# Performance work log

Measured on AMD Instinct MI355X. Metric: run time of the kernel, lower is better.

Reference implementation:

```python
import jax, jax.numpy as jnp
import numpy as np

N_NODES = 50000
N_EDGES = 600000
N_RELS = 19
D_IN = 128
D_HID = 64
D_OUT = 2


def setup_inputs() -> dict:
    key = jax.random.key(0)
    ks = jax.random.split(key, 10)
    feat = jax.random.normal(ks[0], (N_NODES, D_IN), dtype=jnp.float32)
    src = jax.random.randint(ks[1], (N_EDGES,), 0, N_NODES)
    dst = jax.random.randint(ks[2], (N_EDGES,), 0, N_NODES)
    etype = jax.random.randint(ks[3], (N_EDGES,), 0, N_RELS)
    s1 = 1.0 / np.sqrt(D_IN)
    s2 = 1.0 / np.sqrt(D_HID)
    W1 = jax.random.normal(ks[4], (N_RELS, D_IN, D_HID), dtype=jnp.float32) * s1
    loop1 = jax.random.normal(ks[5], (D_IN, D_HID), dtype=jnp.float32) * s1
    b1 = jnp.zeros((D_HID,), dtype=jnp.float32)
    W2 = jax.random.normal(ks[6], (N_RELS, D_HID, D_OUT), dtype=jnp.float32) * s2
    loop2 = jax.random.normal(ks[7], (D_HID, D_OUT), dtype=jnp.float32) * s2
    b2 = jnp.zeros((D_OUT,), dtype=jnp.float32)
    return {"feat": feat, "W1": W1, "loop1": loop1, "b1": b1,
            "W2": W2, "loop2": loop2, "b2": b2,
            "src": src, "dst": dst, "etype": etype}


def _rel_graph_conv(h, W, loop_w, bias, src, dst, etype, activation):
    # Per-relation transform of all nodes: [N, R, O]; then gather per edge.
    # (num_rels * out_feat is small, so this is cheaper than gathering W per edge.)
    transformed = jnp.einsum('nd,rdo->nro', h, W)
    msg = transformed[src, etype]                      # [E, O] edge messages
    agg = jax.ops.segment_sum(msg, dst, num_segments=h.shape[0])  # scatter-add
    out = agg + h @ loop_w + bias                      # self-loop + bias
    if activation is not None:
        out = activation(out)
    return out


def reference(feat, W1, loop1, b1, W2, loop2, b2, src, dst, etype):
    h = _rel_graph_conv(feat, W1, loop1, b1, src, dst, etype, jax.nn.relu)
    h = _rel_graph_conv(h, W2, loop2, b2, src, dst, etype, None)
    return h
```

## Files before the change

kernel.cpp:

```cpp
#include <hip/hip_runtime.h>

#define N_NODES 50000
#define N_EDGES 600000
#define N_RELS  19
#define D_IN    128
#define D_HID   64
#define D_OUT   2
#define BSH     9
#define NB      ((N_NODES + 511) >> 9)
#define NSEG    (NB * N_RELS)
#define NTILE_CAP (NSEG + (N_EDGES + 127) / 128)
#define SL_BLOCKS  ((N_NODES + 63) / 64)
#define PREP_ELEMS (N_RELS * D_HID * D_IN + 48 * 64 + D_HID * D_IN)
#define PREP_BLOCKS ((PREP_ELEMS + 255) / 256)

typedef unsigned short u16;
typedef unsigned int   u32;
typedef __attribute__((ext_vector_type(8))) short sfrag;
typedef __attribute__((ext_vector_type(4))) float f32x4;

__device__ __forceinline__ u16 f2bf(float f){
  union { float f; u32 i; } v; v.f = f;
  u32 r = v.i + 0x7fffu + ((v.i >> 16) & 1u);
  return (u16)(r >> 16);
}
__device__ __forceinline__ float bf2f(u16 u){
  union { u32 i; float f; } v; v.i = ((u32)u) << 16; return v.f;
}
__device__ __forceinline__ u32 pack2(float lo, float hi){
  return (u32)f2bf(lo) | ((u32)f2bf(hi) << 16);
}

__global__ __launch_bounds__(256) void k_fused_pre(const float* __restrict__ feat,
                                                   u16* __restrict__ featb,
                                                   const int* __restrict__ src,
                                                   const int* __restrict__ et,
                                                   const int* __restrict__ dst,
                                                   int* __restrict__ seg_hist,
                                                   int* __restrict__ hist_dst){
  int i = blockIdx.x * 256 + threadIdx.x;
  float2 f = ((const float2*)feat)[i];
  ((u32*)featb)[i] = (u32)f2bf(f.x) | ((u32)f2bf(f.y) << 16);
  if (i < N_EDGES) {
    int key = (src[i] >> BSH) * N_RELS + et[i];
    atomicAdd(&seg_hist[key * 16], 1);
    atomicAdd(&hist_dst[dst[i]], 1);
  }
}

__global__ __launch_bounds__(256) void k_alloc_scan(
    const int* __restrict__ hist_dst, int* __restrict__ dstart,
    int* __restrict__ cur_dst, int* __restrict__ gcnt,
    const int* __restrict__ seg_hist, int* __restrict__ seg_off,
    int* __restrict__ cur_seg, int* __restrict__ ntile,
    int* __restrict__ tseg, int* __restrict__ tstart,
    const float* __restrict__ W1, const float* __restrict__ loop1,
    const float* __restrict__ W2, u16* __restrict__ W1Tb,
    u16* __restrict__ loop1Tb, u16* __restrict__ W2allT){
  if (blockIdx.x >= 197) {
    int idx = (blockIdx.x - 197) * 256 + threadIdx.x;
    const int T1 = N_RELS * D_HID * D_IN;
    const int T2c = T1 + 48 * 64;
    const int T3 = T2c + D_HID * D_IN;
    if (idx < T1) {
      int r = idx / (D_HID * D_IN);
      int t = idx - r * (D_HID * D_IN);
      int j = t >> 7, d = t & 127;
      W1Tb[idx] = f2bf(W1[(r * D_IN + d) * D_HID + j]);
    } else if (idx < T2c) {
      int k2 = idx - T1;
      int n = k2 >> 6, k = k2 & 63;
      float val = 0.f;
      if (n < N_RELS * D_OUT) {
        int r = n >> 1, o = n & 1;
        val = W2[(r * D_HID + k) * D_OUT + o];
      }
      W2allT[k2] = f2bf(val);
    } else if (idx < T3) {
      int k2 = idx - T2c;
      int j = k2 >> 7, d = k2 & 127;
      loop1Tb[k2] = f2bf(loop1[d * D_HID + j]);
    }
    return;
  }
  if (blockIdx.x == 196) {
    __shared__ int se_s[256], st_s[256];
    int tid = threadIdx.x;
    const int PER = (NSEG + 255) / 256;
    int lo = tid * PER, hi = lo + PER; if (hi > NSEG) hi = NSEG; if (lo > NSEG) lo = NSEG;
    int se = 0, st = 0;
    for (int i = lo; i < hi; ++i) { int c = seg_hist[i * 16]; se += c; st += (c + 127) >> 7; }
    se_s[tid] = se; st_s[tid] = st;
    __syncthreads();
    if (tid == 0) {
      int a = 0, b = 0;
      for (int j = 0; j < 256; ++j) { int x = se_s[j], y = st_s[j]; se_s[j] = a; st_s[j] = b; a += x; b += y; }
      ntile[0] = b;
    }
    __syncthreads();
    int eo = se_s[tid], to = st_s[tid];
    for (int i = lo; i < hi; ++i) {
      int c = seg_hist[i * 16];
      seg_off[i] = eo; cur_seg[i * 16] = eo;
      int nt = (c + 127) >> 7;
      for (int k = 0; k < nt; ++k) { tseg[to + k] = i; tstart[to + k] = eo + (k << 7); }
      eo += c; to += nt;
    }
    if (hi == NSEG) seg_off[NSEG] = eo;
    return;
  }
  __shared__ int wbase[4];
  int tid = threadIdx.x, lane = tid & 63, wv = tid >> 6;
  int n = blockIdx.x * 256 + tid;
  int v = (n < N_NODES) ? hist_dst[n] : 0;
  int x = v;
  #pragma unroll
  for (int o = 1; o < 64; o <<= 1) { int u = __shfl_up(x, o); if (lane >= o) x += u; }
  if (lane == 63) wbase[wv] = atomicAdd(gcnt, x);
  __syncthreads();
  int start = wbase[wv] + x - v;
  if (n < N_NODES) { dstart[n] = start; cur_dst[n] = start; }
}

__global__ __launch_bounds__(256) void k_scatter(const int* __restrict__ src,
                                                 const int* __restrict__ et,
                                                 int* __restrict__ cur_seg,
                                                 int* __restrict__ perm){
  int e = blockIdx.x * 256 + threadIdx.x;
  if (e >= N_EDGES) return;
  int key = (src[e] >> BSH) * N_RELS + et[e];
  int p = atomicAdd(&cur_seg[key * 16], 1);
  perm[p] = e;
}

__global__ __launch_bounds__(256) void k_se1(
    const u16* __restrict__ featb, const u16* __restrict__ W1Tb,
    const u16* __restrict__ loop1Tb, const float* __restrict__ b1,
    const int* __restrict__ src, const int* __restrict__ dst,
    const int* __restrict__ perm, const int* __restrict__ seg_off,
    const int* __restrict__ ntile_p, const int* __restrict__ tseg,
    const int* __restrict__ tstart, int* __restrict__ cur_dst,
    int* __restrict__ srel, u16* __restrict__ msgbuf, u16* __restrict__ agg1b){
  __shared__ __align__(16) u16 Bls[64][136];
  __shared__ __align__(16) u16 msg[128][72];
  __shared__ int posIds[128];
  int tid = threadIdx.x, lane = tid & 63, w = tid >> 6;
  int r16 = lane & 15, c4 = lane >> 4;

  if (blockIdx.x >= NTILE_CAP) {
    int base = (blockIdx.x - NTILE_CAP) * 64;
    { int j = tid >> 2, seg = tid & 3;
      const uint4* g = (const uint4*)(loop1Tb + j * 128) + seg * 4;
      uint4* d = (uint4*)&Bls[j][seg * 32];
      d[0] = g[0]; d[1] = g[1]; d[2] = g[2]; d[3] = g[3]; }
    int arow = base + w * 16 + r16; if (arow >= N_NODES) arow = N_NODES - 1;
    sfrag aF[4];
    #pragma unroll
    for (int kk = 0; kk < 4; ++kk)
      aF[kk] = *(const sfrag*)(featb + (size_t)arow * D_IN + kk * 32 + c4 * 8);
    __syncthreads();
    #pragma unroll
    for (int ct = 0; ct < 4; ++ct) {
      f32x4 acc = {0.f, 0.f, 0.f, 0.f};
      #pragma unroll
      for (int kk = 0; kk < 4; ++kk) {
        sfrag bF = *(const sfrag*)&Bls[ct * 16 + r16][kk * 32 + c4 * 8];
        acc = __builtin_amdgcn_mfma_f32_16x16x32_bf16(aF[kk], bF, acc, 0, 0, 0);
      }
      int col = ct * 16 + r16;
      float bias = b1[col];
      #pragma unroll
      for (int reg = 0; reg < 4; ++reg) {
        float v = acc[reg] + bias;
        float o = __shfl_xor(v, 1);
        if (!(lane & 1)) {
          int orow = w * 16 + c4 * 4 + reg;
          *(u32*)&msg[orow][col] = pack2(v, o);
        }
      }
    }
    __syncthreads();
    { int row = tid >> 2, q = tid & 3;
      int n = base + row;
      if (n < N_NODES) {
        uint4 a0 = ((const uint4*)&msg[row][0])[q * 2];
        uint4 a1 = ((const uint4*)&msg[row][0])[q * 2 + 1];
        uint4* d = (uint4*)(agg1b + (size_t)n * D_HID + q * 16);
        d[0] = a0; d[1] = a1;
      } }
    return;
  }

  int nt = *ntile_p;
  int pb = blockIdx.x;
  if (pb >= nt) return;
  int q8 = nt >> 3, r8 = nt & 7;
  int xcd = pb & 7, idx = pb >> 3;
  int b = (xcd < r8 ? xcd * (q8 + 1) : r8 * (q8 + 1) + (xcd - r8) * q8) + idx;

  int seg = tseg[b];
  int ts  = tstart[b];
  int vc  = seg_off[seg + 1] - ts; if (vc > 128) vc = 128;
  int rel = seg % N_RELS;

  int myPos = -1;
  if (tid < 128 && tid < vc) {
    int e = perm[ts + tid];
    int s2 = src[e];
    myPos = atomicAdd(&cur_dst[dst[e]], 1);
    srel[myPos] = (s2 << 5) | rel;
  }
  {
    int j = tid >> 2, seg2 = tid & 3;
    const uint4* g = (const uint4*)(W1Tb + ((size_t)rel * 64 + j) * 128) + seg2 * 4;
    uint4* d = (uint4*)&Bls[j][seg2 * 32];
    d[0] = g[0]; d[1] = g[1]; d[2] = g[2]; d[3] = g[3];
  }
  sfrag aF[2][4];
  #pragma unroll
  for (int mt = 0; mt < 2; ++mt) {
    int row = w * 32 + mt * 16 + r16;
    int rr = row < vc ? row : vc - 1;
    int s = src[perm[ts + rr]];
    const u16* ap = featb + (size_t)s * D_IN + c4 * 8;
    #pragma unroll
    for (int kk = 0; kk < 4; ++kk)
      aF[mt][kk] = *(const sfrag*)(ap + kk * 32);
  }
  __syncthreads();
  #pragma unroll
  for (int ct = 0; ct < 4; ++ct) {
    sfrag bF[4];
    #pragma unroll
    for (int kk = 0; kk < 4; ++kk)
      bF[kk] = *(const sfrag*)&Bls[ct * 16 + r16][kk * 32 + c4 * 8];
    #pragma unroll
    for (int mt = 0; mt < 2; ++mt) {
      f32x4 acc = {0.f, 0.f, 0.f, 0.f};
      #pragma unroll
      for (int kk = 0; kk < 4; ++kk)
        acc = __builtin_amdgcn_mfma_f32_16x16x32_bf16(aF[mt][kk], bF[kk], acc, 0, 0, 0);
      #pragma unroll
      for (int reg = 0; reg < 4; ++reg) {
        float v = acc[reg];
        float o = __shfl_xor(v, 1);
        if (!(lane & 1)) {
          int orow = w * 32 + mt * 16 + c4 * 4 + reg;
          *(u32*)&msg[orow][ct * 16 + r16] = pack2(v, o);
        }
      }
    }
  }
  if (tid < 128) posIds[tid] = myPos;
  __syncthreads();
  { int row = tid >> 1, half = tid & 1;
    int pos = posIds[row];
    if (pos >= 0) {
      const uint4* mr = (const uint4*)&msg[row][half * 32];
      uint4* d = (uint4*)(msgbuf + (size_t)pos * D_HID + half * 32);
      d[0] = mr[0]; d[1] = mr[1]; d[2] = mr[2]; d[3] = mr[3];
    } }
}

__global__ __launch_bounds__(256) void k_agg_relu_self2(
    const u16* __restrict__ msgbuf, const int* __restrict__ dstart,
    const int* __restrict__ cnt, const u16* __restrict__ agg1b,
    const float* __restrict__ loop2, const float* __restrict__ b2,
    u16* __restrict__ h1b, float* __restrict__ out){
  int wv = threadIdx.x >> 6, lane = threadIdx.x & 63;
  int n = blockIdx.x * 4 + wv;
  int s = dstart[n], epos = s + cnt[n];
  int h = lane >> 5, c = lane & 31;
  float a0 = 0.f, a1 = 0.f;
  for (int i = s + h; i < epos; i += 2) {
    u32 v = ((const u32*)msgbuf)[(size_t)i * 32 + c];
    a0 += bf2f((u16)(v & 0xffffu));
    a1 += bf2f((u16)(v >> 16));
  }
  a0 += __shfl_down(a0, 32);
  a1 += __shfl_down(a1, 32);
  float p0 = 0.f, p1 = 0.f;
  if (h == 0) {
    u32 sv = ((const u32*)agg1b)[(size_t)n * 32 + c];
    float v0 = a0 + bf2f((u16)(sv & 0xffffu));
    float v1 = a1 + bf2f((u16)(sv >> 16));
    v0 = v0 > 0.f ? v0 : 0.f;
    v1 = v1 > 0.f ? v1 : 0.f;
    ((u32*)h1b)[(size_t)n * 32 + c] = (u32)f2bf(v0) | ((u32)f2bf(v1) << 16);
    float2 w0 = ((const float2*)loop2)[2 * c];
    float2 w1 = ((const float2*)loop2)[2 * c + 1];
    p0 = v0 * w0.x + v1 * w1.x;
    p1 = v0 * w0.y + v1 * w1.y;
  }
  #pragma unroll
  for (int off = 16; off; off >>= 1) {
    p0 += __shfl_down(p0, off);
    p1 += __shfl_down(p1, off);
  }
  if (lane == 0) {
    out[n * 2]     = p0 + b2[0];
    out[n * 2 + 1] = p1 + b2[1];
  }
}

__global__ __launch_bounds__(256) void k_t2(
    const u16* __restrict__ h1b, const u16* __restrict__ W2allT,
    float* __restrict__ T2){
  __shared__ __align__(16) u16 Bls[48][72];
  int tid = threadIdx.x, lane = tid & 63, w = tid >> 6;
  int r16 = lane & 15, c4 = lane >> 4;
  for (int idx = tid; idx < 48 * 8; idx += 256) {
    int row = idx >> 3, q = idx & 7;
    ((uint4*)&Bls[row][0])[q] = ((const uint4*)W2allT)[idx];
  }
  int base = blockIdx.x * 64;
  int arow = base + w * 16 + r16; if (arow >= N_NODES) arow = N_NODES - 1;
  sfrag aF[2];
  #pragma unroll
  for (int kk = 0; kk < 2; ++kk)
    aF[kk] = *(const sfrag*)(h1b + (size_t)arow * D_HID + kk * 32 + c4 * 8);
  __syncthreads();
  #pragma unroll
  for (int ct = 0; ct < 3; ++ct) {
    f32x4 acc = {0.f, 0.f, 0.f, 0.f};
    #pragma unroll
    for (int kk = 0; kk < 2; ++kk) {
      sfrag bF = *(const sfrag*)&Bls[ct * 16 + r16][kk * 32 + c4 * 8];
      acc = __builtin_amdgcn_mfma_f32_16x16x32_bf16(aF[kk], bF, acc, 0, 0, 0);
    }
    int col = ct * 16 + r16;
    if (col < N_RELS * D_OUT) {
      #pragma unroll
      for (int reg = 0; reg < 4; ++reg) {
        int orow = base + w * 16 + c4 * 4 + reg;
        if (orow < N_NODES) T2[(size_t)orow * 40 + col] = acc[reg];
      }
    }
  }
}

__global__ __launch_bounds__(256) void k_fin(
    const float* __restrict__ T2, const int* __restrict__ srel,
    const int* __restrict__ dstart, const int* __restrict__ cnt,
    float* __restrict__ out){
  int wv = threadIdx.x >> 6, lane = threadIdx.x & 63;
  int n = blockIdx.x * 4 + wv;
  int s = dstart[n], c = cnt[n];
  float ax = 0.f, ay = 0.f;
  for (int i = lane; i < c; i += 64) {
    int sr = srel[s + i];
    const float* p = T2 + (size_t)(sr >> 5) * 40 + (sr & 31) * 2;
    ax += p[0]; ay += p[1];
  }
  #pragma unroll
  for (int off = 32; off; off >>= 1) {
    ax += __shfl_down(ax, off);
    ay += __shfl_down(ay, off);
  }
  if (lane == 0) {
    out[n * 2]     += ax;
    out[n * 2 + 1] += ay;
  }
}

extern "C" void kernel_launch(void* const* d_in, const int* in_sizes, int n_in,
                              void* d_out, int out_size, void* d_ws, size_t ws_size,
                              hipStream_t stream){
  const float* feat  = (const float*)d_in[0];
  const float* W1    = (const float*)d_in[1];
  const float* loop1 = (const float*)d_in[2];
  const float* b1    = (const float*)d_in[3];
  const float* W2    = (const float*)d_in[4];
  const float* loop2 = (const float*)d_in[5];
  const float* b2    = (const float*)d_in[6];
  const int* src     = (const int*)d_in[7];
  const int* dst     = (const int*)d_in[8];
  const int* et      = (const int*)d_in[9];
  float* out = (float*)d_out;

  char* w = (char*)d_ws;
  u16*   W1Tb     = (u16*)(w);
  u16*   W2allT   = (u16*)(w + 311296);
  u16*   loop1Tb  = (u16*)(w + 317440);
  int*   seg_hist = (int*)(w + 333824);
  int*   gcnt     = (int*)(w + 452992);
  int*   hist_dst = (int*)(w + 453056);
  int*   seg_off  = (int*)(w + 653056);
  int*   cur_seg  = (int*)(w + 660544);
  int*   ntile    = (int*)(w + 779712);
  int*   tseg     = (int*)(w + 779776);
  int*   tstart   = (int*)(w + 806016);
  int*   dstart   = (int*)(w + 832256);
  int*   cur_dst  = (int*)(w + 1032256);
  int*   perm     = (int*)(w + 1232256);
  int*   srel     = (int*)(w + 3632256);
  u16*   featb    = (u16*)(w + 6032256);
  float* T2f      = (float*)(w + 6032256);
  u16*   agg1b    = (u16*)(w + 18832256);
  u16*   h1b      = (u16*)(w + 25232256);
  u16*   msgbuf   = (u16*)(w + 31632256);

  hipMemsetAsync(w + 333824, 0, 319232, stream);
  k_fused_pre     <<<12500, 256, 0, stream>>>(feat, featb, src, et, dst, seg_hist, hist_dst);
  k_alloc_scan    <<<197 + PREP_BLOCKS, 256, 0, stream>>>(
                      hist_dst, dstart, cur_dst, gcnt, seg_hist, seg_off, cur_seg,
                      ntile, tseg, tstart, W1, loop1, W2, W1Tb, loop1Tb, W2allT);
  k_scatter       <<<2344,  256, 0, stream>>>(src, et, cur_seg, perm);
  k_se1           <<<NTILE_CAP + SL_BLOCKS, 256, 0, stream>>>(
                      featb, W1Tb, loop1Tb, b1, src, dst, perm, seg_off, ntile,
                      tseg, tstart, cur_dst, srel, msgbuf, agg1b);
  k_agg_relu_self2<<<12500, 256, 0, stream>>>(msgbuf, dstart, hist_dst, agg1b,
                                              loop2, b2, h1b, out);
  k_t2            <<<SL_BLOCKS, 256, 0, stream>>>(h1b, W2allT, T2f);
  k_fin           <<<12500, 256, 0, stream>>>(T2f, srel, dstart, hist_dst, out);
}
```

Before: 304.7 us.

## Process whole segments per block with register-prefetched gathers, drop tile table

```diff
diff --git a/kernel.cpp b/kernel.cpp
--- a/kernel.cpp
+++ b/kernel.cpp
@@ -9,7 +9,6 @@
 #define BSH     9
 #define NB      ((N_NODES + 511) >> 9)
 #define NSEG    (NB * N_RELS)
-#define NTILE_CAP (NSEG + (N_EDGES + 127) / 128)
 #define SL_BLOCKS  ((N_NODES + 63) / 64)
 #define PREP_ELEMS (N_RELS * D_HID * D_IN + 48 * 64 + D_HID * D_IN)
 #define PREP_BLOCKS ((PREP_ELEMS + 255) / 256)
@@ -39,8 +38,9 @@
                                                    int* __restrict__ seg_hist,
                                                    int* __restrict__ hist_dst){
   int i = blockIdx.x * 256 + threadIdx.x;
-  float2 f = ((const float2*)feat)[i];
-  ((u32*)featb)[i] = (u32)f2bf(f.x) | ((u32)f2bf(f.y) << 16);
+  float4 f = ((const float4*)feat)[i];
+  uint2 p; p.x = pack2(f.x, f.y); p.y = pack2(f.z, f.w);
+  ((uint2*)featb)[i] = p;
   if (i < N_EDGES) {
     int key = (src[i] >> BSH) * N_RELS + et[i];
     atomicAdd(&seg_hist[key * 16], 1);
@@ -52,8 +52,7 @@
     const int* __restrict__ hist_dst, int* __restrict__ dstart,
     int* __restrict__ cur_dst, int* __restrict__ gcnt,
     const int* __restrict__ seg_hist, int* __restrict__ seg_off,
-    int* __restrict__ cur_seg, int* __restrict__ ntile,
-    int* __restrict__ tseg, int* __restrict__ tstart,
+    int* __restrict__ cur_seg,
     const float* __restrict__ W1, const float* __restrict__ loop1,
     const float* __restrict__ W2, u16* __restrict__ W1Tb,
     u16* __restrict__ loop1Tb, u16* __restrict__ W2allT){
@@ -84,27 +83,24 @@
     return;
   }
   if (blockIdx.x == 196) {
-    __shared__ int se_s[256], st_s[256];
+    __shared__ int se_s[256];
     int tid = threadIdx.x;
     const int PER = (NSEG + 255) / 256;
     int lo = tid * PER, hi = lo + PER; if (hi > NSEG) hi = NSEG; if (lo > NSEG) lo = NSEG;
-    int se = 0, st = 0;
-    for (int i = lo; i < hi; ++i) { int c = seg_hist[i * 16]; se += c; st += (c + 127) >> 7; }
-    se_s[tid] = se; st_s[tid] = st;
+    int se = 0;
+    for (int i = lo; i < hi; ++i) se += seg_hist[i * 16];
+    se_s[tid] = se;
     __syncthreads();
     if (tid == 0) {
-      int a = 0, b = 0;
-      for (int j = 0; j < 256; ++j) { int x = se_s[j], y = st_s[j]; se_s[j] = a; st_s[j] = b; a += x; b += y; }
-      ntile[0] = b;
-    }
-    __syncthreads();
-    int eo = se_s[tid], to = st_s[tid];
+      int a = 0;
+      for (int j = 0; j < 256; ++j) { int x = se_s[j]; se_s[j] = a; a += x; }
+    }
+    __syncthreads();
+    int eo = se_s[tid];
     for (int i = lo; i < hi; ++i) {
       int c = seg_hist[i * 16];
       seg_off[i] = eo; cur_seg[i * 16] = eo;
-      int nt = (c + 127) >> 7;
-      for (int k = 0; k < nt; ++k) { tseg[to + k] = i; tstart[to + k] = eo + (k << 7); }
-      eo += c; to += nt;
+      eo += c;
     }
     if (hi == NSEG) seg_off[NSEG] = eo;
     return;
@@ -133,25 +129,49 @@
   perm[p] = e;
 }
 
-__global__ __launch_bounds__(256) void k_se1(
+__device__ __forceinline__ void gather_tile(
+    const u16* __restrict__ featb, const int* __restrict__ src,
+    const int* __restrict__ dst, const int* __restrict__ perm,
+    int* __restrict__ cur_dst, int* __restrict__ srel,
+    int ts, int c, int t0, int rel, int tid, int w, int r16, int c4,
+    sfrag (&aN)[2][4], int& nextPos){
+  int vc = c - t0; if (vc > 128) vc = 128;
+  #pragma unroll
+  for (int mt = 0; mt < 2; ++mt) {
+    int row = w * 32 + mt * 16 + r16;
+    int rr = row < vc ? row : vc - 1;
+    int s = src[perm[ts + t0 + rr]];
+    const u16* ap = featb + (size_t)s * D_IN + c4 * 8;
+    #pragma unroll
+    for (int kk = 0; kk < 4; ++kk)
+      aN[mt][kk] = *(const sfrag*)(ap + kk * 32);
+  }
+  nextPos = -1;
+  if (tid < 128 && tid < vc) {
+    int e = perm[ts + t0 + tid];
+    nextPos = atomicAdd(&cur_dst[dst[e]], 1);
+    srel[nextPos] = (src[e] << 5) | rel;
+  }
+}
+
+__global__ __launch_bounds__(256, 4) void k_se1(
     const u16* __restrict__ featb, const u16* __restrict__ W1Tb,
     const u16* __restrict__ loop1Tb, const float* __restrict__ b1,
     const int* __restrict__ src, const int* __restrict__ dst,
     const int* __restrict__ perm, const int* __restrict__ seg_off,
-    const int* __restrict__ ntile_p, const int* __restrict__ tseg,
-    const int* __restrict__ tstart, int* __restrict__ cur_dst,
-    int* __restrict__ srel, u16* __restrict__ msgbuf, u16* __restrict__ agg1b){
+    int* __restrict__ cur_dst, int* __restrict__ srel,
+    u16* __restrict__ msgbuf, u16* __restrict__ agg1b){
   __shared__ __align__(16) u16 Bls[64][136];
   __shared__ __align__(16) u16 msg[128][72];
   __shared__ int posIds[128];
   int tid = threadIdx.x, lane = tid & 63, w = tid >> 6;
   int r16 = lane & 15, c4 = lane >> 4;
 
-  if (blockIdx.x >= NTILE_CAP) {
-    int base = (blockIdx.x - NTILE_CAP) * 64;
-    { int j = tid >> 2, seg = tid & 3;
-      const uint4* g = (const uint4*)(loop1Tb + j * 128) + seg * 4;
-      uint4* d = (uint4*)&Bls[j][seg * 32];
+  if (blockIdx.x >= NSEG) {
+    int base = (blockIdx.x - NSEG) * 64;
+    { int j = tid >> 2, sg = tid & 3;
+      const uint4* g = (const uint4*)(loop1Tb + j * 128) + sg * 4;
+      uint4* d = (uint4*)&Bls[j][sg * 32];
       d[0] = g[0]; d[1] = g[1]; d[2] = g[2]; d[3] = g[3]; }
     int arow = base + w * 16 + r16; if (arow >= N_NODES) arow = N_NODES - 1;
     sfrag aF[4];
@@ -191,75 +211,69 @@
     return;
   }
 
-  int nt = *ntile_p;
-  int pb = blockIdx.x;
-  if (pb >= nt) return;
-  int q8 = nt >> 3, r8 = nt & 7;
-  int xcd = pb & 7, idx = pb >> 3;
-  int b = (xcd < r8 ? xcd * (q8 + 1) : r8 * (q8 + 1) + (xcd - r8) * q8) + idx;
-
-  int seg = tseg[b];
-  int ts  = tstart[b];
-  int vc  = seg_off[seg + 1] - ts; if (vc > 128) vc = 128;
-  int rel = seg % N_RELS;
-
-  int myPos = -1;
-  if (tid < 128 && tid < vc) {
-    int e = perm[ts + tid];
-    int s2 = src[e];
-    myPos = atomicAdd(&cur_dst[dst[e]], 1);
-    srel[myPos] = (s2 << 5) | rel;
-  }
+  const int q8 = NSEG >> 3, r8 = NSEG & 7;
+  int xcd = blockIdx.x & 7, cidx = blockIdx.x >> 3;
+  int seg = (xcd < r8 ? xcd * (q8 + 1) : r8 * (q8 + 1) + (xcd - r8) * q8) + cidx;
+  int ts = seg_off[seg], c = seg_off[seg + 1] - ts;
+  if (c == 0) return;
+  int rel = seg - (seg / N_RELS) * N_RELS;
+
   {
-    int j = tid >> 2, seg2 = tid & 3;
-    const uint4* g = (const uint4*)(W1Tb + ((size_t)rel * 64 + j) * 128) + seg2 * 4;
-    uint4* d = (uint4*)&Bls[j][seg2 * 32];
+    int j = tid >> 2, sg = tid & 3;
+    const uint4* g = (const uint4*)(W1Tb + ((size_t)rel * 64 + j) * 128) + sg * 4;
+    uint4* d = (uint4*)&Bls[j][sg * 32];
     d[0] = g[0]; d[1] = g[1]; d[2] = g[2]; d[3] = g[3];
   }
-  sfrag aF[2][4];
-  #pragma unroll
-  for (int mt = 0; mt < 2; ++mt) {
-    int row = w * 32 + mt * 16 + r16;
-    int rr = row < vc ? row : vc - 1;
-    int s = src[perm[ts + rr]];
-    const u16* ap = featb + (size_t)s * D_IN + c4 * 8;
-    #pragma unroll
-    for (int kk = 0; kk < 4; ++kk)
-      aF[mt][kk] = *(const sfrag*)(ap + kk * 32);
-  }
+
+  sfrag aN[2][4]; int nextPos;
+  gather_tile(featb, src, dst, perm, cur_dst, srel, ts, c, 0, rel,
+              tid, w, r16, c4, aN, nextPos);
   __syncthreads();
-  #pragma unroll
-  for (int ct = 0; ct < 4; ++ct) {
-    sfrag bF[4];
-    #pragma unroll
-    for (int kk = 0; kk < 4; ++kk)
-      bF[kk] = *(const sfrag*)&Bls[ct * 16 + r16][kk * 32 + c4 * 8];
-    #pragma unroll
-    for (int mt = 0; mt < 2; ++mt) {
-      f32x4 acc = {0.f, 0.f, 0.f, 0.f};
+
+  for (int t0 = 0; t0 < c; t0 += 128) {
+    sfrag aC[2][4];
+    #pragma unroll
+    for (int mt = 0; mt < 2; ++mt)
+      #pragma unroll
+      for (int kk = 0; kk < 4; ++kk) aC[mt][kk] = aN[mt][kk];
+    int curPos = nextPos;
+    if (t0 + 128 < c)
+      gather_tile(featb, src, dst, perm, cur_dst, srel, ts, c, t0 + 128, rel,
+                  tid, w, r16, c4, aN, nextPos);
+    #pragma unroll
+    for (int ct = 0; ct < 4; ++ct) {
+      sfrag bF[4];
       #pragma unroll
       for (int kk = 0; kk < 4; ++kk)
-        acc = __builtin_amdgcn_mfma_f32_16x16x32_bf16(aF[mt][kk], bF[kk], acc, 0, 0, 0);
-      #pragma unroll
-      for (int reg = 0; reg < 4; ++reg) {
-        float v = acc[reg];
-        float o = __shfl_xor(v, 1);
-        if (!(lane & 1)) {
-          int orow = w * 32 + mt * 16 + c4 * 4 + reg;
-          *(u32*)&msg[orow][ct * 16 + r16] = pack2(v, o);
+        bF[kk] = *(const sfrag*)&Bls[ct * 16 + r16][kk * 32 + c4 * 8];
+      #pragma unroll
+      for (int mt = 0; mt < 2; ++mt) {
+        f32x4 acc = {0.f, 0.f, 0.f, 0.f};
+        #pragma unroll
+        for (int kk = 0; kk < 4; ++kk)
+          acc = __builtin_amdgcn_mfma_f32_16x16x32_bf16(aC[mt][kk], bF[kk], acc, 0, 0, 0);
+        #pragma unroll
+        for (int reg = 0; reg < 4; ++reg) {
+          float v = acc[reg];
+          float o = __shfl_xor(v, 1);
+          if (!(lane & 1)) {
+            int orow = w * 32 + mt * 16 + c4 * 4 + reg;
+            *(u32*)&msg[orow][ct * 16 + r16] = pack2(v, o);
+          }
         }
       }
     }
-  }
-  if (tid < 128) posIds[tid] = myPos;
-  __syncthreads();
-  { int row = tid >> 1, half = tid & 1;
-    int pos = posIds[row];
-    if (pos >= 0) {
-      const uint4* mr = (const uint4*)&msg[row][half * 32];
-      uint4* d = (uint4*)(msgbuf + (size_t)pos * D_HID + half * 32);
-      d[0] = mr[0]; d[1] = mr[1]; d[2] = mr[2]; d[3] = mr[3];
-    } }
+    if (tid < 128) posIds[tid] = curPos;
+    __syncthreads();
+    { int row = tid >> 1, half = tid & 1;
+      int pos = posIds[row];
+      if (pos >= 0) {
+        const uint4* mr = (const uint4*)&msg[row][half * 32];
+        uint4* d = (uint4*)(msgbuf + (size_t)pos * D_HID + half * 32);
+        d[0] = mr[0]; d[1] = mr[1]; d[2] = mr[2]; d[3] = mr[3];
+      } }
+    __syncthreads();
+  }
 }
 
 __global__ __launch_bounds__(256) void k_agg_relu_self2(
@@ -387,28 +401,25 @@
   int*   hist_dst = (int*)(w + 453056);
   int*   seg_off  = (int*)(w + 653056);
   int*   cur_seg  = (int*)(w + 660544);
-  int*   ntile    = (int*)(w + 779712);
-  int*   tseg     = (int*)(w + 779776);
-  int*   tstart   = (int*)(w + 806016);
-  int*   dstart   = (int*)(w + 832256);
-  int*   cur_dst  = (int*)(w + 1032256);
-  int*   perm     = (int*)(w + 1232256);
-  int*   srel     = (int*)(w + 3632256);
-  u16*   featb    = (u16*)(w + 6032256);
-  float* T2f      = (float*)(w + 6032256);
-  u16*   agg1b    = (u16*)(w + 18832256);
-  u16*   h1b      = (u16*)(w + 25232256);
-  u16*   msgbuf   = (u16*)(w + 31632256);
+  int*   dstart   = (int*)(w + 779712);
+  int*   cur_dst  = (int*)(w + 979712);
+  int*   perm     = (int*)(w + 1179712);
+  int*   srel     = (int*)(w + 3579712);
+  u16*   featb    = (u16*)(w + 5979712);
+  float* T2f      = (float*)(w + 5979712);
+  u16*   agg1b    = (u16*)(w + 18779712);
+  u16*   h1b      = (u16*)(w + 25179712);
+  u16*   msgbuf   = (u16*)(w + 31579712);
 
   hipMemsetAsync(w + 333824, 0, 319232, stream);
-  k_fused_pre     <<<12500, 256, 0, stream>>>(feat, featb, src, et, dst, seg_hist, hist_dst);
+  k_fused_pre     <<<6250, 256, 0, stream>>>(feat, featb, src, et, dst, seg_hist, hist_dst);
   k_alloc_scan    <<<197 + PREP_BLOCKS, 256, 0, stream>>>(
                       hist_dst, dstart, cur_dst, gcnt, seg_hist, seg_off, cur_seg,
-                      ntile, tseg, tstart, W1, loop1, W2, W1Tb, loop1Tb, W2allT);
+                      W1, loop1, W2, W1Tb, loop1Tb, W2allT);
   k_scatter       <<<2344,  256, 0, stream>>>(src, et, cur_seg, perm);
-  k_se1           <<<NTILE_CAP + SL_BLOCKS, 256, 0, stream>>>(
-                      featb, W1Tb, loop1Tb, b1, src, dst, perm, seg_off, ntile,
-                      tseg, tstart, cur_dst, srel, msgbuf, agg1b);
+  k_se1           <<<NSEG + SL_BLOCKS, 256, 0, stream>>>(
+                      featb, W1Tb, loop1Tb, b1, src, dst, perm, seg_off,
+                      cur_dst, srel, msgbuf, agg1b);
   k_agg_relu_self2<<<12500, 256, 0, stream>>>(msgbuf, dstart, hist_dst, agg1b,
                                               loop2, b2, h1b, out);
   k_t2            <<<SL_BLOCKS, 256, 0, stream>>>(h1b, W2allT, T2f);
```

Result: no change. 302.4 us (-0.8%).
